# Performance work log

Measured on AMD Instinct MI355X. Metric: run time of the kernel, lower is better.

Reference implementation:

```python
import jax, jax.numpy as jnp
import numpy as np

VOCAB, EMBED, HIDDEN, LAYERS = 256, 32, 32, 10
B, T = 1024, 1024


def setup_inputs() -> dict:
    key = jax.random.key(0)
    ks = jax.random.split(key, 8)
    s_e = 1.0  # nn.Embedding default init is N(0,1); scale others like uniform fan-in
    k_rnn = 1.0 / np.sqrt(HIDDEN)
    k_fc = 1.0 / np.sqrt(HIDDEN)
    x = jax.random.randint(ks[0], (B, T), 0, VOCAB, dtype=jnp.int64) if jax.config.jax_enable_x64 else jax.random.randint(ks[0], (B, T), 0, VOCAB, dtype=jnp.int32)
    emb = jax.random.normal(ks[1], (VOCAB, EMBED), dtype=jnp.float32) * s_e
    W_ih = jax.random.uniform(ks[2], (LAYERS, HIDDEN, EMBED), jnp.float32, -k_rnn, k_rnn)
    W_hh = jax.random.uniform(ks[3], (LAYERS, HIDDEN, HIDDEN), jnp.float32, -k_rnn, k_rnn)
    b_ih = jax.random.uniform(ks[4], (LAYERS, HIDDEN), jnp.float32, -k_rnn, k_rnn)
    b_hh = jax.random.uniform(ks[5], (LAYERS, HIDDEN), jnp.float32, -k_rnn, k_rnn)
    W_fc = jax.random.uniform(ks[6], (VOCAB, HIDDEN), jnp.float32, -k_fc, k_fc)
    b_fc = jax.random.uniform(ks[7], (VOCAB,), jnp.float32, -k_fc, k_fc)
    return {"x": x, "emb": emb, "W_ih": W_ih, "W_hh": W_hh,
            "b_ih": b_ih, "b_hh": b_hh, "W_fc": W_fc, "b_fc": b_fc}


def reference(x, emb, W_ih, W_hh, b_ih, b_hh, W_fc, b_fc):
    # Embedding lookup: [B, T, E]
    xe = emb[x]
    L = W_ih.shape[0]
    Bn = x.shape[0]
    h0 = jnp.zeros((L, Bn, W_hh.shape[-1]), dtype=xe.dtype)

    def step(h, xt):
        # h: [L, B, H]; xt: [B, E]
        inp = xt
        new_h = []
        for l in range(L):  # sequential across layers (true dependency)
            hl = jnp.tanh(inp @ W_ih[l].T + b_ih[l] + h[l] @ W_hh[l].T + b_hh[l])
            new_h.append(hl)
            inp = hl
        return jnp.stack(new_h), None

    hT, _ = jax.lax.scan(step, h0, jnp.swapaxes(xe, 0, 1))  # scan over T
    # out[:, -1, :] of top RNN layer == final hidden of last layer
    return hT[-1] @ W_fc.T + b_fc
```

## Files before the change

kernel.cpp:

```cpp
#include <hip/hip_runtime.h>

#define VOCABSZ 256
#define EMBED   32
#define HIDDEN  32
#define LAYERS  10
#define BATCH   1024
#define SEQ     1024
#define BPB     16
#define U       4
#define NITER   (SEQ / U + LAYERS - 1)

typedef _Float16 f16x8 __attribute__((ext_vector_type(8)));
typedef float    f32x4 __attribute__((ext_vector_type(4)));
typedef _Float16 h2    __attribute__((ext_vector_type(2)));

__device__ __forceinline__ unsigned pk(float a, float b) {
    h2 t; t[0] = (_Float16)a; t[1] = (_Float16)b;
    return __builtin_bit_cast(unsigned, t);
}
__device__ __forceinline__ f16x8 u2f(uint4 u) { return __builtin_bit_cast(f16x8, u); }

__global__ __launch_bounds__(640, 1) void rnn_mfma(
    const int* __restrict__ x, const float* __restrict__ emb,
    const float* __restrict__ W_ih, const float* __restrict__ W_hh,
    const float* __restrict__ b_ih, const float* __restrict__ b_hh,
    float* __restrict__ h_out)
{
    __shared__ unsigned xl[(SEQ / 4) * BPB];
    __shared__ __align__(16) unsigned char hb[2 * LAYERS * U * 1024];

    const int tid   = threadIdx.x;
    const int w     = tid >> 6;
    const int lane  = tid & 63;
    const int bc    = lane & 15;
    const int g     = lane >> 4;
    const int bbase = blockIdx.x * BPB;

    const int4* xg4 = (const int4*)(x + bbase * SEQ);
    for (int i = tid; i < (SEQ / 4) * BPB; i += 640) {
        const int4 v = xg4[i];
        xl[(i & 255) * BPB + (i >> 8)] =
            (unsigned)(v.x | (v.y << 8) | (v.z << 16) | (v.w << 24));
    }
    for (int i = tid; i < (int)sizeof(hb) / 4; i += 640)
        ((unsigned*)hb)[i] = 0u;

    f16x8 wf00, wf01, wf10, wf11;
    {
        const float4* p00 = (const float4*)(W_ih + (w * HIDDEN + bc)      * EMBED  + g * 8);
        const float4* p10 = (const float4*)(W_ih + (w * HIDDEN + 16 + bc) * EMBED  + g * 8);
        const float4* p01 = (const float4*)(W_hh + (w * HIDDEN + bc)      * HIDDEN + g * 8);
        const float4* p11 = (const float4*)(W_hh + (w * HIDDEN + 16 + bc) * HIDDEN + g * 8);
        float4 a, b;
        a = p00[0]; b = p00[1];
        wf00 = u2f(uint4{pk(a.x, a.y), pk(a.z, a.w), pk(b.x, b.y), pk(b.z, b.w)});
        a = p01[0]; b = p01[1];
        wf01 = u2f(uint4{pk(a.x, a.y), pk(a.z, a.w), pk(b.x, b.y), pk(b.z, b.w)});
        a = p10[0]; b = p10[1];
        wf10 = u2f(uint4{pk(a.x, a.y), pk(a.z, a.w), pk(b.x, b.y), pk(b.z, b.w)});
        a = p11[0]; b = p11[1];
        wf11 = u2f(uint4{pk(a.x, a.y), pk(a.z, a.w), pk(b.x, b.y), pk(b.z, b.w)});
    }
    float bias[8];
    #pragma unroll
    for (int m = 0; m < 2; ++m)
        #pragma unroll
        for (int r = 0; r < 4; ++r) {
            const int hid = w * HIDDEN + m * 16 + g * 4 + r;
            bias[m * 4 + r] = b_ih[hid] + b_hh[hid];
        }

    #define SL(p, l, u) ((((p) * LAYERS + (l)) * U + (u)) * 1024)
    const int rd_off  = g * 256 + bc * 16;
    const int wr_off0 = (g >> 1) * 256 + bc * 16 + (g & 1) * 8;
    const int wr_off1 = wr_off0 + 512;

    __syncthreads();

    uint4  cur[U];
    float4 eraw[U][2];
    if (w == 0) {
        const unsigned gw = xl[0 * BPB + bc];
        #pragma unroll
        for (int u = 0; u < U; ++u) {
            const int tok = (gw >> (8 * u)) & 255;
            const float4* ep = (const float4*)(emb + tok * EMBED + g * 8);
            const float4 e0 = ep[0], e1 = ep[1];
            cur[u] = uint4{pk(e0.x, e0.y), pk(e0.z, e0.w), pk(e1.x, e1.y), pk(e1.z, e1.w)};
        }
    }

    auto body = [&](int it, int P) {
        __syncthreads();
        const int tb = (it - w) * U;
        if (tb < 0 || tb >= SEQ) return;

        const bool pf = (w == 0) && (tb + U < SEQ);
        if (pf) {
            const unsigned gw = xl[((tb + U) >> 2) * BPB + bc];
            #pragma unroll
            for (int u = 0; u < U; ++u) {
                const int tok = (gw >> (8 * u)) & 255;
                const float4* ep = (const float4*)(emb + tok * EMBED + g * 8);
                eraw[u][0] = ep[0]; eraw[u][1] = ep[1];
            }
        }

        uint4 bin[U];
        if (w == 0) {
            #pragma unroll
            for (int u = 0; u < U; ++u) bin[u] = cur[u];
        } else {
            #pragma unroll
            for (int u = 0; u < U; ++u)
                bin[u] = *(const uint4*)(hb + SL(P ^ 1, w - 1, u) + rd_off);
        }
        uint4 bown = *(const uint4*)(hb + SL(P ^ 1, w, U - 1) + rd_off);

        #pragma unroll
        for (int u = 0; u < U; ++u) {
            f32x4 c0 = {0.f, 0.f, 0.f, 0.f}, c1 = {0.f, 0.f, 0.f, 0.f};
            c0 = __builtin_amdgcn_mfma_f32_16x16x32_f16(wf00, u2f(bin[u]), c0, 0, 0, 0);
            c1 = __builtin_amdgcn_mfma_f32_16x16x32_f16(wf10, u2f(bin[u]), c1, 0, 0, 0);
            c0 = __builtin_amdgcn_mfma_f32_16x16x32_f16(wf01, u2f(bown),   c0, 0, 0, 0);
            c1 = __builtin_amdgcn_mfma_f32_16x16x32_f16(wf11, u2f(bown),   c1, 0, 0, 0);

            float hv[8];
            #pragma unroll
            for (int r = 0; r < 4; ++r) {
                {
                    const float a  = c0[r] + bias[r];
                    const float e  = __expf(a + a);
                    const float rc = __builtin_amdgcn_rcpf(1.0f + e);
                    hv[r] = 1.0f - (rc + rc);
                }
                {
                    const float a  = c1[r] + bias[4 + r];
                    const float e  = __expf(a + a);
                    const float rc = __builtin_amdgcn_rcpf(1.0f + e);
                    hv[4 + r] = 1.0f - (rc + rc);
                }
            }

            const int sb = SL(P, w, u);
            *(uint2*)(hb + sb + wr_off0) = uint2{pk(hv[0], hv[1]), pk(hv[2], hv[3])};
            *(uint2*)(hb + sb + wr_off1) = uint2{pk(hv[4], hv[5]), pk(hv[6], hv[7])};

            if (u < U - 1)
                bown = *(const uint4*)(hb + sb + rd_off);

            if (w == LAYERS - 1 && tb + u == SEQ - 1) {
                #pragma unroll
                for (int r = 0; r < 4; ++r) {
                    h_out[(bbase + bc) * HIDDEN + g * 4 + r]      = hv[r];
                    h_out[(bbase + bc) * HIDDEN + 16 + g * 4 + r] = hv[4 + r];
                }
            }
        }

        if (pf) {
            #pragma unroll
            for (int u = 0; u < U; ++u) {
                const float4 e0 = eraw[u][0], e1 = eraw[u][1];
                cur[u] = uint4{pk(e0.x, e0.y), pk(e0.z, e0.w), pk(e1.x, e1.y), pk(e1.z, e1.w)};
            }
        }
    };

    for (int it = 0; it < NITER + 1; it += 2) {
        body(it, 0);
        body(it + 1, 1);
    }
    #undef SL
}

__global__ __launch_bounds__(256) void rnn_fc(
    const float* __restrict__ h_fin, const float* __restrict__ W_fc,
    const float* __restrict__ b_fc, float* __restrict__ out)
{
    const int b = blockIdx.x;
    const int v = threadIdx.x;
    const float4* hr = (const float4*)(h_fin + b * HIDDEN);
    const float4* wr = (const float4*)(W_fc + v * HIDDEN);
    float acc = b_fc[v];
    #pragma unroll
    for (int c = 0; c < 8; ++c) {
        const float4 hv = hr[c], wv = wr[c];
        acc += hv.x * wv.x + hv.y * wv.y + hv.z * wv.z + hv.w * wv.w;
    }
    out[b * VOCABSZ + v] = acc;
}

extern "C" void kernel_launch(void* const* d_in, const int* in_sizes, int n_in,
                              void* d_out, int out_size, void* d_ws, size_t ws_size,
                              hipStream_t stream) {
    const int*   x    = (const int*)d_in[0];
    const float* emb  = (const float*)d_in[1];
    const float* W_ih = (const float*)d_in[2];
    const float* W_hh = (const float*)d_in[3];
    const float* b_ih = (const float*)d_in[4];
    const float* b_hh = (const float*)d_in[5];
    const float* W_fc = (const float*)d_in[6];
    const float* b_fc = (const float*)d_in[7];
    float* out   = (float*)d_out;
    float* h_fin = (float*)d_ws;

    rnn_mfma<<<BATCH / BPB, 640, 0, stream>>>(x, emb, W_ih, W_hh, b_ih, b_hh, h_fin);
    rnn_fc<<<BATCH, VOCABSZ, 0, stream>>>(h_fin, W_fc, b_fc, out);
}
```

Baseline: 617.1 us.

## Keep recurrent state in registers via K-permuted weights, hoist input MFMAs

Permutes the K ordering of the W_hh (and non-first-layer W_ih) fragments so each lane's packed MFMA output can be fed straight back as the B operand. The own-layer hidden state then stays in registers instead of round-tripping through LDS every timestep. The input-projection MFMAs for all U steps are issued ahead of the serial recurrent chain, and tanh is folded into a single fma+exp2 with a pre-scaled bias. Tokens are now read directly from global memory with a one-step-ahead prefetch, which drops the LDS token staging and the initial barrier. The risk is extra global-load latency on the layer-0 wave and added register pressure.

Measured after the change: 535.0 us. -13.3%, faster.

```diff
diff --git a/kernel.cpp b/kernel.cpp
--- a/kernel.cpp
+++ b/kernel.cpp
@@ -20,13 +20,34 @@
 }
 __device__ __forceinline__ f16x8 u2f(uint4 u) { return __builtin_bit_cast(f16x8, u); }
 
+__device__ __forceinline__ float th(float c, float b2) {
+    const float t = __builtin_fmaf(c, 2.8853900817779268f, b2);
+#if __has_builtin(__builtin_amdgcn_exp2f)
+    const float e = __builtin_amdgcn_exp2f(t);
+#else
+    const float e = __expf(0.6931471805599453f * t);
+#endif
+    const float r = __builtin_amdgcn_rcpf(1.0f + e);
+    return __builtin_fmaf(-2.0f, r, 1.0f);
+}
+
+__device__ __forceinline__ uint4 mk_nat(const float* row, int g) {
+    const float4 a = *(const float4*)(row + 8 * g);
+    const float4 b = *(const float4*)(row + 8 * g + 4);
+    return uint4{pk(a.x, a.y), pk(a.z, a.w), pk(b.x, b.y), pk(b.z, b.w)};
+}
+__device__ __forceinline__ uint4 mk_kp(const float* row, int g) {
+    const float4 a = *(const float4*)(row + 4 * g);
+    const float4 b = *(const float4*)(row + 16 + 4 * g);
+    return uint4{pk(a.x, a.y), pk(a.z, a.w), pk(b.x, b.y), pk(b.z, b.w)};
+}
+
 __global__ __launch_bounds__(640, 1) void rnn_mfma(
     const int* __restrict__ x, const float* __restrict__ emb,
     const float* __restrict__ W_ih, const float* __restrict__ W_hh,
     const float* __restrict__ b_ih, const float* __restrict__ b_hh,
     float* __restrict__ h_out)
 {
-    __shared__ unsigned xl[(SEQ / 4) * BPB];
     __shared__ __align__(16) unsigned char hb[2 * LAYERS * U * 1024];
 
     const int tid   = threadIdx.x;
@@ -36,59 +57,46 @@
     const int g     = lane >> 4;
     const int bbase = blockIdx.x * BPB;
 
-    const int4* xg4 = (const int4*)(x + bbase * SEQ);
-    for (int i = tid; i < (SEQ / 4) * BPB; i += 640) {
-        const int4 v = xg4[i];
-        xl[(i & 255) * BPB + (i >> 8)] =
-            (unsigned)(v.x | (v.y << 8) | (v.z << 16) | (v.w << 24));
-    }
     for (int i = tid; i < (int)sizeof(hb) / 4; i += 640)
         ((unsigned*)hb)[i] = 0u;
 
-    f16x8 wf00, wf01, wf10, wf11;
-    {
-        const float4* p00 = (const float4*)(W_ih + (w * HIDDEN + bc)      * EMBED  + g * 8);
-        const float4* p10 = (const float4*)(W_ih + (w * HIDDEN + 16 + bc) * EMBED  + g * 8);
-        const float4* p01 = (const float4*)(W_hh + (w * HIDDEN + bc)      * HIDDEN + g * 8);
-        const float4* p11 = (const float4*)(W_hh + (w * HIDDEN + 16 + bc) * HIDDEN + g * 8);
-        float4 a, b;
-        a = p00[0]; b = p00[1];
-        wf00 = u2f(uint4{pk(a.x, a.y), pk(a.z, a.w), pk(b.x, b.y), pk(b.z, b.w)});
-        a = p01[0]; b = p01[1];
-        wf01 = u2f(uint4{pk(a.x, a.y), pk(a.z, a.w), pk(b.x, b.y), pk(b.z, b.w)});
-        a = p10[0]; b = p10[1];
-        wf10 = u2f(uint4{pk(a.x, a.y), pk(a.z, a.w), pk(b.x, b.y), pk(b.z, b.w)});
-        a = p11[0]; b = p11[1];
-        wf11 = u2f(uint4{pk(a.x, a.y), pk(a.z, a.w), pk(b.x, b.y), pk(b.z, b.w)});
-    }
-    float bias[8];
+    const float* ri0 = W_ih + (w * HIDDEN + bc)      * EMBED;
+    const float* ri1 = W_ih + (w * HIDDEN + 16 + bc) * EMBED;
+    const float* rh0 = W_hh + (w * HIDDEN + bc)      * HIDDEN;
+    const float* rh1 = W_hh + (w * HIDDEN + 16 + bc) * HIDDEN;
+    const uint4 wf00 = (w == 0) ? mk_nat(ri0, g) : mk_kp(ri0, g);
+    const uint4 wf10 = (w == 0) ? mk_nat(ri1, g) : mk_kp(ri1, g);
+    const uint4 wf01 = mk_kp(rh0, g);
+    const uint4 wf11 = mk_kp(rh1, g);
+
+    float bias2[8];
     #pragma unroll
     for (int m = 0; m < 2; ++m)
         #pragma unroll
         for (int r = 0; r < 4; ++r) {
             const int hid = w * HIDDEN + m * 16 + g * 4 + r;
-            bias[m * 4 + r] = b_ih[hid] + b_hh[hid];
+            bias2[m * 4 + r] = 2.8853900817779268f * (b_ih[hid] + b_hh[hid]);
         }
 
     #define SL(p, l, u) ((((p) * LAYERS + (l)) * U + (u)) * 1024)
-    const int rd_off  = g * 256 + bc * 16;
-    const int wr_off0 = (g >> 1) * 256 + bc * 16 + (g & 1) * 8;
-    const int wr_off1 = wr_off0 + 512;
-
-    __syncthreads();
+    const int off = g * 256 + bc * 16;
 
     uint4  cur[U];
     float4 eraw[U][2];
+    int4   tok_pf;
     if (w == 0) {
-        const unsigned gw = xl[0 * BPB + bc];
+        const int4 t4 = *(const int4*)(x + (bbase + bc) * SEQ);
+        const int tk[U] = {t4.x, t4.y, t4.z, t4.w};
         #pragma unroll
         for (int u = 0; u < U; ++u) {
-            const int tok = (gw >> (8 * u)) & 255;
-            const float4* ep = (const float4*)(emb + tok * EMBED + g * 8);
+            const float4* ep = (const float4*)(emb + tk[u] * EMBED + g * 8);
             const float4 e0 = ep[0], e1 = ep[1];
             cur[u] = uint4{pk(e0.x, e0.y), pk(e0.z, e0.w), pk(e1.x, e1.y), pk(e1.z, e1.w)};
         }
+        tok_pf = *(const int4*)(x + (bbase + bc) * SEQ + U);
     }
+
+    uint4 bown = uint4{0, 0, 0, 0};
 
     auto body = [&](int it, int P) {
         __syncthreads();
@@ -97,13 +105,14 @@
 
         const bool pf = (w == 0) && (tb + U < SEQ);
         if (pf) {
-            const unsigned gw = xl[((tb + U) >> 2) * BPB + bc];
+            const int tk[U] = {tok_pf.x, tok_pf.y, tok_pf.z, tok_pf.w};
             #pragma unroll
             for (int u = 0; u < U; ++u) {
-                const int tok = (gw >> (8 * u)) & 255;
-                const float4* ep = (const float4*)(emb + tok * EMBED + g * 8);
+                const float4* ep = (const float4*)(emb + tk[u] * EMBED + g * 8);
                 eraw[u][0] = ep[0]; eraw[u][1] = ep[1];
             }
+            if (tb + 2 * U < SEQ)
+                tok_pf = *(const int4*)(x + (bbase + bc) * SEQ + tb + 2 * U);
         }
 
         uint4 bin[U];
@@ -113,41 +122,32 @@
         } else {
             #pragma unroll
             for (int u = 0; u < U; ++u)
-                bin[u] = *(const uint4*)(hb + SL(P ^ 1, w - 1, u) + rd_off);
-        }
-        uint4 bown = *(const uint4*)(hb + SL(P ^ 1, w, U - 1) + rd_off);
-
+                bin[u] = *(const uint4*)(hb + SL(P ^ 1, w - 1, u) + off);
+        }
+        f32x4 cin0[U], cin1[U];
+        const f32x4 z = {0.f, 0.f, 0.f, 0.f};
         #pragma unroll
         for (int u = 0; u < U; ++u) {
-            f32x4 c0 = {0.f, 0.f, 0.f, 0.f}, c1 = {0.f, 0.f, 0.f, 0.f};
-            c0 = __builtin_amdgcn_mfma_f32_16x16x32_f16(wf00, u2f(bin[u]), c0, 0, 0, 0);
-            c1 = __builtin_amdgcn_mfma_f32_16x16x32_f16(wf10, u2f(bin[u]), c1, 0, 0, 0);
-            c0 = __builtin_amdgcn_mfma_f32_16x16x32_f16(wf01, u2f(bown),   c0, 0, 0, 0);
-            c1 = __builtin_amdgcn_mfma_f32_16x16x32_f16(wf11, u2f(bown),   c1, 0, 0, 0);
+            cin0[u] = __builtin_amdgcn_mfma_f32_16x16x32_f16(u2f(wf00), u2f(bin[u]), z, 0, 0, 0);
+            cin1[u] = __builtin_amdgcn_mfma_f32_16x16x32_f16(u2f(wf10), u2f(bin[u]), z, 0, 0, 0);
+        }
+
+        #pragma unroll
+        for (int u = 0; u < U; ++u) {
+            const f32x4 c0 = __builtin_amdgcn_mfma_f32_16x16x32_f16(u2f(wf01), u2f(bown), cin0[u], 0, 0, 0);
+            const f32x4 c1 = __builtin_amdgcn_mfma_f32_16x16x32_f16(u2f(wf11), u2f(bown), cin1[u], 0, 0, 0);
 
             float hv[8];
             #pragma unroll
             for (int r = 0; r < 4; ++r) {
-                {
-                    const float a  = c0[r] + bias[r];
-                    const float e  = __expf(a + a);
-                    const float rc = __builtin_amdgcn_rcpf(1.0f + e);
-                    hv[r] = 1.0f - (rc + rc);
-                }
-                {
-                    const float a  = c1[r] + bias[4 + r];
-                    const float e  = __expf(a + a);
-                    const float rc = __builtin_amdgcn_rcpf(1.0f + e);
-                    hv[4 + r] = 1.0f - (rc + rc);
-                }
-            }
-
-            const int sb = SL(P, w, u);
-            *(uint2*)(hb + sb + wr_off0) = uint2{pk(hv[0], hv[1]), pk(hv[2], hv[3])};
-            *(uint2*)(hb + sb + wr_off1) = uint2{pk(hv[4], hv[5]), pk(hv[6], hv[7])};
-
-            if (u < U - 1)
-                bown = *(const uint4*)(hb + sb + rd_off);
+                hv[r]     = th(c0[r], bias2[r]);
+                hv[4 + r] = th(c1[r], bias2[4 + r]);
+            }
+            bown = uint4{pk(hv[0], hv[1]), pk(hv[2], hv[3]),
+                         pk(hv[4], hv[5]), pk(hv[6], hv[7])};
+
+            if (w < LAYERS - 1)
+                *(uint4*)(hb + SL(P, w, u) + off) = bown;
 
             if (w == LAYERS - 1 && tb + u == SEQ - 1) {
                 #pragma unroll
```
